# Performance work log

Measured on AMD Instinct MI355X. Metric: run time of the kernel, lower is better.

## Reference

```python
import jax, jax.numpy as jnp
import numpy as np

EXPAND = 2
KCONV = 4


def _mamba(x, Win, Wconv, bconv, Wx, Wdt, bdt, Alog, Dskip, Wout):
    # x: (B, C, H, W) -> flatten HW to a sequence, run Mamba (S6) block, reshape back
    B, C, H, W = x.shape
    L = H * W
    Di, Kc = Wconv.shape
    R = Wdt.shape[0]
    N = Alog.shape[1]
    xl = x.reshape(B, C, L).transpose(0, 2, 1)            # (B, L, C)
    xz = xl @ Win                                          # (B, L, 2*Di)
    xs, z = xz[..., :Di], xz[..., Di:]
    xt = xs.transpose(0, 2, 1)                             # (B, Di, L)
    xp = jnp.pad(xt, ((0, 0), (0, 0), (Kc - 1, 0)))        # causal depthwise conv1d
    conv = bconv[None, :, None]
    for k in range(Kc):
        conv = conv + Wconv[:, k][None, :, None] * xp[:, :, k:k + L]
    u = jax.nn.silu(conv).transpose(0, 2, 1)               # (B, L, Di)
    dbc = u @ Wx                                           # (B, L, R+2N)
    dt = jax.nn.softplus(dbc[..., :R] @ Wdt + bdt)         # (B, L, Di)
    Bm = dbc[..., R:R + N]                                 # (B, L, N)
    Cm = dbc[..., R + N:]                                  # (B, L, N)
    A = -jnp.exp(Alog)                                     # (Di, N)
    dA = jnp.exp(dt[..., None] * A)                        # (B, L, Di, N)
    dBx = dt[..., None] * Bm[:, :, None, :] * u[..., None] # (B, L, Di, N)

    def step(h, inp):
        a, bx, c = inp
        h = a * h + bx
        return h, jnp.einsum('bdn,bn->bd', h, c)

    h0 = jnp.zeros((B, Di, N), x.dtype)
    _, ys = jax.lax.scan(step, h0, (jnp.swapaxes(dA, 0, 1), jnp.swapaxes(dBx, 0, 1), jnp.swapaxes(Cm, 0, 1)))
    y = jnp.swapaxes(ys, 0, 1) + u * Dskip                 # (B, L, Di)
    y = y * jax.nn.silu(z)
    return (y @ Wout).transpose(0, 2, 1).reshape(B, C, H, W)


def _resize_bilinear(x, oh, ow):
    # F.interpolate(mode='bilinear', align_corners=True)
    B, C, H, W = x.shape
    ys = jnp.linspace(0.0, H - 1.0, oh)
    xs = jnp.linspace(0.0, W - 1.0, ow)
    y0 = jnp.floor(ys).astype(jnp.int32); y1 = jnp.clip(y0 + 1, 0, H - 1); wy = (ys - y0)[:, None]
    x0 = jnp.floor(xs).astype(jnp.int32); x1 = jnp.clip(x0 + 1, 0, W - 1); wx = (xs - x0)[None, :]
    r0 = x[:, :, y0, :]
    r1 = x[:, :, y1, :]
    top = r0[..., x0] * (1 - wx) + r0[..., x1] * wx
    bot = r1[..., x0] * (1 - wx) + r1[..., x1] * wx
    return top * (1 - wy) + bot * wy


def _mamba_params(key, D, N):
    Di = EXPAND * D
    R = max(1, D // 16)
    ks = jax.random.split(key, 6)
    s = 0.02
    Win = s * jax.random.normal(ks[0], (D, 2 * Di), jnp.float32)
    Wconv = s * jax.random.normal(ks[1], (Di, KCONV), jnp.float32)
    bconv = jnp.zeros((Di,), jnp.float32)
    Wx = s * jax.random.normal(ks[2], (Di, R + 2 * N), jnp.float32)
    Wdt = s * jax.random.normal(ks[3], (R, Di), jnp.float32)
    bdt = s * jax.random.normal(ks[4], (Di,), jnp.float32)
    Alog = jnp.tile(jnp.log(jnp.arange(1, N + 1, dtype=jnp.float32))[None, :], (Di, 1))
    Dskip = jnp.ones((Di,), jnp.float32)
    Wout = s * jax.random.normal(ks[5], (Di, D), jnp.float32)
    return Win, Wconv, bconv, Wx, Wdt, bdt, Alog, Dskip, Wout


def setup_inputs() -> dict:
    key = jax.random.key(0)
    C, B, N = 64, 2, 16
    sizes = [48, 24, 12, 6]
    ks = jax.random.split(key, 16)
    inp = {}
    for i, s in enumerate(sizes):
        inp[f'feat{i}'] = jax.random.normal(ks[i], (B, C, s, s), jnp.float32)
    names = ['Win', 'Wconv', 'bconv', 'Wx', 'Wdt', 'bdt', 'Alog', 'D', 'Wout']
    lvl = [_mamba_params(ks[4 + i], C, N) for i in range(4)]
    for j, nm in enumerate(names):
        inp['lvl_' + nm] = jnp.stack([lvl[i][j] for i in range(4)])
    cr = _mamba_params(ks[8], 4 * C, N)
    for j, nm in enumerate(names):
        inp['cr_' + nm] = cr[j]
    inp['proj_W'] = 0.02 * jax.random.normal(ks[9], (C, 4 * C), jnp.float32)  # 1x1 conv weight (out,in)
    inp['proj_b'] = jnp.zeros((C,), jnp.float32)
    inp['bn_g'] = jnp.ones((C,), jnp.float32)
    inp['bn_b'] = jnp.zeros((C,), jnp.float32)
    inp['bn_m'] = 0.1 * jax.random.normal(ks[10], (C,), jnp.float32)
    inp['bn_v'] = jax.random.uniform(ks[11], (C,), jnp.float32, minval=0.5, maxval=1.5)
    inp['target_h'] = 48
    inp['target_w'] = 48
    return inp


def reference(feat0, feat1, feat2, feat3,
              lvl_Win, lvl_Wconv, lvl_bconv, lvl_Wx, lvl_Wdt, lvl_bdt, lvl_Alog, lvl_D, lvl_Wout,
              cr_Win, cr_Wconv, cr_bconv, cr_Wx, cr_Wdt, cr_bdt, cr_Alog, cr_D, cr_Wout,
              proj_W, proj_b, bn_g, bn_b, bn_m, bn_v, target_h, target_w):
    feats = [feat0, feat1, feat2, feat3]
    processed = []
    for i, f in enumerate(feats):
        f = f + _mamba(f, lvl_Win[i], lvl_Wconv[i], lvl_bconv[i], lvl_Wx[i], lvl_Wdt[i],
                       lvl_bdt[i], lvl_Alog[i], lvl_D[i], lvl_Wout[i])
        processed.append(_resize_bilinear(f, target_h, target_w))
    x = jnp.concatenate(processed, axis=1)                 # (B, 4C, th, tw)
    x = x + _mamba(x, cr_Win, cr_Wconv, cr_bconv, cr_Wx, cr_Wdt, cr_bdt, cr_Alog, cr_D, cr_Wout)
    y = jnp.einsum('bchw,oc->bohw', x, proj_W) + proj_b[None, :, None, None]
    scale = (bn_g / jnp.sqrt(bn_v + 1e-5))[None, :, None, None]
    y = (y - bn_m[None, :, None, None]) * scale + bn_b[None, :, None, None]
    return jax.nn.relu(y)
```

## Files before the change

### kernel.cpp

```cpp
#include <hip/hip_runtime.h>
#include <cmath>

#define DEV __device__ __forceinline__

typedef unsigned short u16;
typedef u16 u16x8 __attribute__((ext_vector_type(8)));
typedef u16 u16x4 __attribute__((ext_vector_type(4)));
typedef short bf16x8 __attribute__((ext_vector_type(8)));
typedef float f32x4 __attribute__((ext_vector_type(4)));

constexpr int B_ = 2;
constexpr int S4[4]    = {48, 24, 12, 6};
constexpr int L4[4]    = {2304, 576, 144, 36};
constexpr int LOFF4[4] = {0, 2304, 2880, 3024};
constexpr int LTOT = 3060;
constexpr int TOFF4[4] = {0, 144, 180, 189};
constexpr int NTT = 192;
constexpr int NCH4[4]   = {36, 9, 3, 1};
constexpr int CHOFF4[4] = {0, 36, 45, 48};
constexpr int NCHL = 49;
constexpr int NCHC = 36;
constexpr int LC = 2304;
constexpr float LOG2E = 1.44269504088896f;

DEV float siluf(float x) { return x / (1.f + __expf(-x)); }
DEV float softplusf(float x) { return fmaxf(x, 0.f) + log1pf(__expf(-fabsf(x))); }
DEV float b2f(u16 x) { union { float f; unsigned u; } v; v.u = ((unsigned)x) << 16; return v.f; }
DEV u16 f2b(float f) {
  union { float f; unsigned u; } v; v.f = f;
  unsigned r = v.u + 0x7fffu + ((v.u >> 16) & 1u);
  return (u16)(r >> 16);
}

__global__ __launch_bounds__(256) void k_prep(
    const float* __restrict__ projW, const float* __restrict__ crWout,
    const float* __restrict__ cWin, const float* __restrict__ cWx,
    float* __restrict__ Wt, float* __restrict__ WP,
    u16* __restrict__ WinT, float* __restrict__ WxT) {
  __shared__ float sm[64 * 65];
  int blk = blockIdx.x;
  int tid = threadIdx.x;
  if (blk < 64) {
    int i = blk * 256 + tid;
    int o = i >> 8, c = i & 255;
    Wt[c * 64 + o] = projW[o * 256 + c];
  } else if (blk < 192) {
    int i = (blk - 64) * 256 + tid;
    int d = i >> 6, o = i & 63;
    float acc = 0.f;
#pragma unroll 4
    for (int c = 0; c < 256; ++c)
      acc = fmaf(crWout[d * 256 + c], projW[o * 256 + c], acc);
    WP[d * 64 + o] = acc;
  } else if (blk < 256) {
    int t = blk - 192;
    int ct = t & 3, nt = t >> 2;
    int c0 = ct * 64, n0 = nt * 64;
    for (int i = tid; i < 4096; i += 256) {
      int cc = i >> 6, nn = i & 63;
      sm[cc * 65 + nn] = cWin[(size_t)(c0 + cc) * 1024 + n0 + nn];
    }
    __syncthreads();
    for (int i = tid; i < 4096; i += 256) {
      int nn = i >> 6, cc = i & 63;
      WinT[(size_t)(n0 + nn) * 256 + c0 + cc] = f2b(sm[cc * 65 + nn]);
    }
  } else {
    int i = (blk - 256) * 256 + tid;
    int d = i & 511, j = i >> 9;
    WxT[j * 512 + d] = cWx[d * 48 + j];
  }
}

__global__ __launch_bounds__(256) void k_front_lvl(
    const float* __restrict__ f0, const float* __restrict__ f1,
    const float* __restrict__ f2, const float* __restrict__ f3,
    const float* __restrict__ Win,
    const float* __restrict__ Wconv,
    const float* __restrict__ bconv,
    const float* __restrict__ Wx,
    const float* __restrict__ Wdt,
    const float* __restrict__ bdt,
    u16* __restrict__ u_l, u16* __restrict__ dt_l,
    u16* __restrict__ Bm_l, u16* __restrict__ Cm_l, u16* __restrict__ z_l) {
  __shared__ float s_x[64 * 20];
  __shared__ float s_xs[19 * 128];
  __shared__ float s_u[16 * 132];
  __shared__ float s_dbc[16 * 36];
  int bid = blockIdx.x;
  int b = bid / NTT, t = bid - b * NTT;
  int lvl = 0;
  while (lvl < 3 && t >= TOFF4[lvl + 1]) ++lvl;
  int tl = t - TOFF4[lvl];
  int L = L4[lvl], loff = LOFF4[lvl];
  int l0 = tl * 16;
  int nl = min(16, L - l0);
  const float* fx = lvl == 0 ? f0 : lvl == 1 ? f1 : lvl == 2 ? f2 : f3;
  int tid = threadIdx.x;

  for (int i = tid; i < 64 * 20; i += 256) {
    int c = i / 20, r = i - c * 20;
    int l = l0 - 3 + r;
    float v = 0.f;
    if (r < 19 && l >= 0 && l < L) v = fx[(size_t)(b * 64 + c) * L + l];
    s_x[i] = v;
  }
  __syncthreads();
  {
    int j = tid;
    float acc[19];
#pragma unroll
    for (int r = 0; r < 19; ++r) acc[r] = 0.f;
    const float* W = Win + lvl * 64 * 256 + j;
    for (int c = 0; c < 64; ++c) {
      float w = W[c * 256];
#pragma unroll
      for (int r = 0; r < 19; ++r) acc[r] = fmaf(w, s_x[c * 20 + r], acc[r]);
    }
    if (j < 128) {
#pragma unroll
      for (int r = 0; r < 19; ++r) s_xs[r * 128 + j] = acc[r];
    } else {
      int d = j - 128;
      int dti = d >> 4, jj = d & 15;
      for (int r = 3; r < 19; ++r) {
        int l = l0 - 3 + r;
        if (l < l0 + nl)
          z_l[((size_t)(b * 8 + dti) * LTOT + loff + l) * 16 + jj] = f2b(acc[r]);
      }
    }
  }
  __syncthreads();
  for (int i = tid; i < 16 * 128; i += 256) {
    int l = i >> 7, d = i & 127;
    if (l < nl) {
      const float* wc = Wconv + (lvl * 128 + d) * 4;
      float a = bconv[lvl * 128 + d];
#pragma unroll
      for (int k = 0; k < 4; ++k) a = fmaf(wc[k], s_xs[(l + k) * 128 + d], a);
      float uu = siluf(a);
      s_u[l * 132 + d] = uu;
      u_l[((size_t)(b * 8 + (d >> 4)) * LTOT + loff + l0 + l) * 16 + (d & 15)] = f2b(uu);
    }
  }
  __syncthreads();
  for (int i = tid; i < 16 * 36; i += 256) {
    int l = i & 15, jj = i >> 4;
    if (l < nl) {
      const float* wx = Wx + lvl * 128 * 36 + jj;
      float a = 0.f;
      for (int d = 0; d < 128; ++d) a = fmaf(s_u[l * 132 + d], wx[d * 36], a);
      s_dbc[l * 36 + jj] = a;
      if (jj >= 4) {
        int q = jj - 4;
        size_t gb = ((size_t)(b * LTOT) + loff + l0 + l) * 16;
        if (q < 16) Bm_l[gb + q] = f2b(a);
        else        Cm_l[gb + (q - 16)] = f2b(a);
      }
    }
  }
  __syncthreads();
  for (int i = tid; i < 16 * 128; i += 256) {
    int l = i >> 7, d = i & 127;
    if (l < nl) {
      float a = bdt[lvl * 128 + d];
#pragma unroll
      for (int r = 0; r < 4; ++r)
        a = fmaf(s_dbc[l * 36 + r], Wdt[(lvl * 4 + r) * 128 + d], a);
      dt_l[((size_t)(b * 8 + (d >> 4)) * LTOT + loff + l0 + l) * 16 + (d & 15)] =
          f2b(softplusf(a));
    }
  }
}

template <int MODE, int PASSC>
__global__ __launch_bounds__(256) void k_scan(
    const u16* __restrict__ dtb, const u16* __restrict__ ub,
    const u16* __restrict__ Bmb, const u16* __restrict__ Cmb,
    const u16* __restrict__ zb,
    const float* __restrict__ Alog, const float* __restrict__ Dsk,
    float* __restrict__ hloc, float* __restrict__ Ssum,
    const float* __restrict__ hin, u16* __restrict__ yg) {
  constexpr int DI = MODE ? 512 : 128;
  constexpr int NDT = DI / 16;
  constexpr int NB = DI / 64;
  constexpr int NCHT = MODE ? NCHC : NCHL;
  constexpr int LT = MODE ? LC : LTOT;
  __shared__ __align__(16) u16 smem[PASSC ? 14336 : 9216];
  u16* s_dt = smem;
  u16* s_u  = smem + 4096;
  u16* s_B  = smem + 8192;
  u16* s_C  = PASSC ? smem + 9216 : nullptr;
  u16* s_y  = PASSC ? smem + 10240 : nullptr;

  int bid = blockIdx.x;
  int dblk = bid % NB;
  int rem = bid / NB;
  int gc = rem % NCHT;
  int b = rem / NCHT;
  int lvl = 0, ch = gc, Lq = LC, loff = 0;
  if (MODE == 0) {
    while (lvl < 3 && gc >= CHOFF4[lvl + 1]) ++lvl;
    ch = gc - CHOFF4[lvl];
    Lq = L4[lvl];
    loff = LOFF4[lvl];
  }
  int l0 = ch * 64;
  int len = min(64, Lq - l0);
  int labs0 = loff + l0;
  int tid = threadIdx.x;
  int q = tid & 3;
  int dl = (tid >> 2) & 15;
  int ti_l = tid >> 6;
  int dti = dblk * 4 + ti_l;
  int d = dti * 16 + dl;
  int n0 = q * 4;

  for (int ti = 0; ti < 4; ++ti) {
    size_t g2 = ((size_t)(b * NDT + dblk * 4 + ti) * LT + labs0) * 16;
    const u16x8* pdt = (const u16x8*)(dtb + g2);
    const u16x8* pu  = (const u16x8*)(ub + g2);
    for (int i = tid; i < len * 2; i += 256) {
      *(u16x8*)&s_dt[ti * 1024 + i * 8] = pdt[i];
      *(u16x8*)&s_u [ti * 1024 + i * 8] = pu[i];
    }
  }
  {
    size_t gB = ((size_t)b * LT + labs0) * 16;
    for (int i = tid; i < len * 2; i += 256) {
      *(u16x8*)&s_B[i * 8] = *(const u16x8*)&Bmb[gB + i * 8];
      if (PASSC) *(u16x8*)&s_C[i * 8] = *(const u16x8*)&Cmb[gB + i * 8];
    }
  }
  __syncthreads();

  int ai = (MODE ? d : lvl * 128 + d);
  float4 al = *(const float4*)&Alog[ai * 16 + n0];
  float kA2[4] = {-__expf(al.x) * LOG2E, -__expf(al.y) * LOG2E,
                  -__expf(al.z) * LOG2E, -__expf(al.w) * LOG2E};
  size_t hix = (((size_t)(b * NCHT) + gc) * DI + d) * 16 + n0;
  float h[4] = {0.f, 0.f, 0.f, 0.f};
  if (PASSC) {
    float4 hv = *(const float4*)&hin[hix];
    h[0] = hv.x; h[1] = hv.y; h[2] = hv.z; h[3] = hv.w;
  }
  float dsk = PASSC ? Dsk[ai] : 0.f;
  float ss = 0.f;

  for (int l = 0; l < len; ++l) {
    float dt = b2f(s_dt[ti_l * 1024 + l * 16 + dl]);
    float uu = b2f(s_u [ti_l * 1024 + l * 16 + dl]);
    float dtu = dt * uu;
    u16x4 Bv = *(const u16x4*)&s_B[l * 16 + n0];
    if (PASSC) {
      u16x4 Cv = *(const u16x4*)&s_C[l * 16 + n0];
      float p = 0.f;
#pragma unroll
      for (int i = 0; i < 4; ++i) {
        float dA = exp2f(kA2[i] * dt);
        h[i] = fmaf(dA, h[i], dtu * b2f(Bv[i]));
        p = fmaf(h[i], b2f(Cv[i]), p);
      }
      p += __shfl_xor(p, 1, 4);
      p += __shfl_xor(p, 2, 4);
      if (q == 0) s_y[l * 64 + ti_l * 16 + dl] = f2b(fmaf(uu, dsk, p));
    } else {
#pragma unroll
      for (int i = 0; i < 4; ++i) {
        float dA = exp2f(kA2[i] * dt);
        h[i] = fmaf(dA, h[i], dtu * b2f(Bv[i]));
      }
      ss += dt;
    }
  }
  if (!PASSC) {
    f32x4 hv = {h[0], h[1], h[2], h[3]};
    *(f32x4*)&hloc[hix] = hv;
    if (q == 0) Ssum[((size_t)(b * NCHT) + gc) * DI + d] = ss;
  } else {
    __syncthreads();
    for (int ti = 0; ti < 4; ++ti) {
      size_t g2 = ((size_t)(b * NDT + dblk * 4 + ti) * LT + labs0) * 16;
      for (int i = tid; i < len * 2; i += 256) {
        u16x8 zv = *(const u16x8*)&zb[g2 + i * 8];
        u16x8 yv = *(const u16x8*)&s_y[(i >> 1) * 64 + ti * 16 + (i & 1) * 8];
        u16x8 o;
#pragma unroll
        for (int j = 0; j < 8; ++j) {
          float z = b2f(zv[j]);
          float gate = z / (1.f + __expf(-z));
          o[j] = f2b(b2f(yv[j]) * gate);
        }
        *(u16x8*)&yg[g2 + i * 8] = o;
      }
    }
  }
}

__global__ __launch_bounds__(256) void k_combine_lvl(
    const float* __restrict__ Alog, const float* __restrict__ hloc,
    const float* __restrict__ Ssum, float* __restrict__ hin) {
  int i = blockIdx.x * 256 + threadIdx.x;
  int n = i & 15, d = (i >> 4) & 127, lvl = (i >> 11) & 3, b = i >> 13;
  float kA2 = -__expf(Alog[(lvl * 128 + d) * 16 + n]) * LOG2E;
  float h = 0.f;
  int nch = NCH4[lvl];
  for (int ch = 0; ch < nch; ++ch) {
    int gc = CHOFF4[lvl] + ch;
    size_t ix = (((size_t)(b * NCHL) + gc) * 128 + d) * 16 + n;
    hin[ix] = h;
    float S = Ssum[((size_t)(b * NCHL) + gc) * 128 + d];
    h = fmaf(exp2f(kA2 * S), h, hloc[ix]);
  }
}

__global__ __launch_bounds__(256) void k_combine_cr(
    const float* __restrict__ Alog, const float* __restrict__ hloc,
    const float* __restrict__ Ssum, float* __restrict__ hin) {
  int i = blockIdx.x * 256 + threadIdx.x;
  int n = i & 15, d = (i >> 4) & 511, b = i >> 13;
  float kA2 = -__expf(Alog[d * 16 + n]) * LOG2E;
  float h = 0.f;
  for (int ch = 0; ch < NCHC; ++ch) {
    size_t ix = (((size_t)(b * NCHC) + ch) * 512 + d) * 16 + n;
    hin[ix] = h;
    float S = Ssum[((size_t)(b * NCHC) + ch) * 512 + d];
    h = fmaf(exp2f(kA2 * S), h, hloc[ix]);
  }
}

__global__ __launch_bounds__(256) void k_out_lvl(
    const u16* __restrict__ yg_l, const float* __restrict__ Wout,
    const float* __restrict__ f0, const float* __restrict__ f1,
    const float* __restrict__ f2, const float* __restrict__ f3,
    float* __restrict__ fout) {
  __shared__ float s_ygT[128 * 20];
  __shared__ float s_o[16 * 64];
  int bid = blockIdx.x;
  int b = bid / NTT, t = bid - b * NTT;
  int lvl = 0;
  while (lvl < 3 && t >= TOFF4[lvl + 1]) ++lvl;
  int tl = t - TOFF4[lvl];
  int L = L4[lvl], loff = LOFF4[lvl];
  int l0 = tl * 16, nl = min(16, L - l0);
  const float* fx = lvl == 0 ? f0 : lvl == 1 ? f1 : lvl == 2 ? f2 : f3;
  int tid = threadIdx.x;
  for (int i = tid; i < 16 * 128; i += 256) {
    int d = i & 127, l = i >> 7;
    float v = 0.f;
    if (l < nl)
      v = b2f(yg_l[((size_t)(b * 8 + (d >> 4)) * LTOT + loff + l0 + l) * 16 + (d & 15)]);
    s_ygT[d * 20 + l] = v;
  }
  __syncthreads();
  {
    int c = tid & 63, lg = (tid >> 6) * 4;
    float acc[4] = {0.f, 0.f, 0.f, 0.f};
    const float* W = Wout + lvl * 128 * 64 + c;
    for (int dq = 0; dq < 128; ++dq) {
      float w = W[dq * 64];
      float4 yv = *(const float4*)&s_ygT[dq * 20 + lg];
      acc[0] = fmaf(w, yv.x, acc[0]);
      acc[1] = fmaf(w, yv.y, acc[1]);
      acc[2] = fmaf(w, yv.z, acc[2]);
      acc[3] = fmaf(w, yv.w, acc[3]);
    }
#pragma unroll
    for (int a = 0; a < 4; ++a) s_o[(lg + a) * 64 + c] = acc[a];
  }
  __syncthreads();
  for (int i = tid; i < 16 * 64; i += 256) {
    int c = i >> 4, l = i & 15;
    if (l < nl)
      fout[((size_t)(b * 64) + c) * LTOT + loff + l0 + l] =
          s_o[l * 64 + c] + fx[((size_t)(b * 64) + c) * L + l0 + l];
  }
}

__global__ __launch_bounds__(256) void k_resize(const float* __restrict__ fout,
                                                float* __restrict__ xTf,
                                                u16* __restrict__ xTb) {
  int i = blockIdx.x * 256 + threadIdx.x;
  int ch = i & 255;
  int rem = i >> 8;
  int hw = rem % 2304;
  int b = rem / 2304;
  int oh = hw / 48, ow = hw - oh * 48;
  int lvl = ch >> 6, c = ch & 63;
  int s = S4[lvl];
  const float* base = fout + ((size_t)(b * 64) + c) * LTOT + LOFF4[lvl];
  float scl = (float)(s - 1) * (1.f / 47.f);
  float fy = oh * scl, fxx = ow * scl;
  int y0 = (int)floorf(fy), x0 = (int)floorf(fxx);
  float wy = fy - y0, wx = fxx - x0;
  int y1 = min(y0 + 1, s - 1), x1 = min(x0 + 1, s - 1);
  float v00 = base[y0 * s + x0], v01 = base[y0 * s + x1];
  float v10 = base[y1 * s + x0], v11 = base[y1 * s + x1];
  float top = v00 * (1.f - wx) + v01 * wx;
  float bot = v10 * (1.f - wx) + v11 * wx;
  float v = top * (1.f - wy) + bot * wy;
  xTf[i] = v;
  xTb[i] = f2b(v);
}

__global__ __launch_bounds__(256) void k_gemm_mfma(
    const u16* __restrict__ xT,
    const u16* __restrict__ WT,
    u16* __restrict__ xs_c, u16* __restrict__ z_c) {
  __shared__ __align__(16) u16 s_a[64 * 72];
  __shared__ __align__(16) u16 s_b[128 * 72];
  int bid = blockIdx.x;
  int nj = bid & 7, bm = bid >> 3;
  int tid = threadIdx.x;
  int lane = tid & 63, w = tid >> 6;
  int wm = (w & 1) * 32, wn = (w >> 1) * 64;
  const int m_base = bm * 64;
  const int n_base = nj * 128;

  f32x4 acc[2][4];
#pragma unroll
  for (int mi = 0; mi < 2; ++mi)
#pragma unroll
    for (int ni = 0; ni < 4; ++ni) acc[mi][ni] = {0.f, 0.f, 0.f, 0.f};

  u16x8 ra0, ra1, rb0, rb1, rb2, rb3;
  auto ld = [&](int c0) {
#pragma unroll
    for (int s = 0; s < 2; ++s) {
      int v = s * 256 + tid;
      int row = v >> 3, kc = (v & 7) * 8;
      u16x8 t = *(const u16x8*)&xT[(size_t)(m_base + row) * 256 + c0 + kc];
      if (s == 0) ra0 = t; else ra1 = t;
    }
#pragma unroll
    for (int s = 0; s < 4; ++s) {
      int v = s * 256 + tid;
      int row = v >> 3, kc = (v & 7) * 8;
      u16x8 t = *(const u16x8*)&WT[(size_t)(n_base + row) * 256 + c0 + kc];
      if (s == 0) rb0 = t; else if (s == 1) rb1 = t;
      else if (s == 2) rb2 = t; else rb3 = t;
    }
  };
  auto st = [&]() {
#pragma unroll
    for (int s = 0; s < 2; ++s) {
      int v = s * 256 + tid;
      int row = v >> 3, kc = (v & 7) * 8;
      *(u16x8*)&s_a[row * 72 + kc] = (s == 0) ? ra0 : ra1;
    }
#pragma unroll
    for (int s = 0; s < 4; ++s) {
      int v = s * 256 + tid;
      int row = v >> 3, kc = (v & 7) * 8;
      const u16x8& t = (s == 0) ? rb0 : (s == 1) ? rb1 : (s == 2) ? rb2 : rb3;
      *(u16x8*)&s_b[row * 72 + kc] = t;
    }
  };
  ld(0);
  int mlane = lane & 15, kg = (lane >> 4) * 8;
  for (int kt = 0; kt < 4; ++kt) {
    st();
    __syncthreads();
    if (kt < 3) ld((kt + 1) * 64);
#pragma unroll
    for (int kk = 0; kk < 2; ++kk) {
      int k0 = kk * 32 + kg;
      bf16x8 af[2], bfr[4];
#pragma unroll
      for (int mi = 0; mi < 2; ++mi)
        af[mi] = *(const bf16x8*)&s_a[(wm + mi * 16 + mlane) * 72 + k0];
#pragma unroll
      for (int ni = 0; ni < 4; ++ni)
        bfr[ni] = *(const bf16x8*)&s_b[(wn + ni * 16 + mlane) * 72 + k0];
#pragma unroll
      for (int mi = 0; mi < 2; ++mi)
#pragma unroll
        for (int ni = 0; ni < 4; ++ni)
          acc[mi][ni] = __builtin_amdgcn_mfma_f32_16x16x32_bf16(
              af[mi], bfr[ni], acc[mi][ni], 0, 0, 0);
    }
    __syncthreads();
  }
  int rgrp = (lane >> 4) * 4;
#pragma unroll
  for (int mi = 0; mi < 2; ++mi) {
#pragma unroll
    for (int ni = 0; ni < 4; ++ni) {
      int n = n_base + wn + ni * 16 + mlane;
#pragma unroll
      for (int r = 0; r < 4; ++r) {
        int gm = m_base + wm + mi * 16 + rgrp + r;
        int b = gm >= 2304;
        int l = gm - b * 2304;
        u16 v = f2b(acc[mi][ni][r]);
        if (n < 512) {
          xs_c[((size_t)(b * LC) + l) * 512 + n] = v;
        } else {
          int dz = n - 512;
          z_c[((size_t)(b * 32 + (dz >> 4)) * LC + l) * 16 + (dz & 15)] = v;
        }
      }
    }
  }
}

__global__ __launch_bounds__(1024) void k_mid_cr(
    const u16* __restrict__ xs_c,
    const float* __restrict__ Wconv,
    const float* __restrict__ bconv,
    const float* __restrict__ WxT,
    const float* __restrict__ Wdt,
    const float* __restrict__ bdt, u16* __restrict__ u_c,
    u16* __restrict__ dt_c, u16* __restrict__ Bm_c, u16* __restrict__ Cm_c) {
  __shared__ __align__(16) u16 s_xs[19 * 512];
  __shared__ __align__(16) u16 s_ub[16 * 520];
  __shared__ __align__(16) float s_wx[48 * 132];
  __shared__ float s_dbc[16 * 48];
  int bid = blockIdx.x;
  int b = bid / 144, tl = bid - b * 144;
  int l0 = tl * 16;
  int tid = threadIdx.x;
  for (int i = tid; i < 19 * 64; i += 1024) {
    int r = i >> 6, c8 = (i & 63) * 8;
    int l = l0 - 3 + r;
    u16x8 v = {0, 0, 0, 0, 0, 0, 0, 0};
    if (l >= 0)
      v = *(const u16x8*)&xs_c[((size_t)(b * LC) + l) * 512 + c8];
    *(u16x8*)&s_xs[r * 512 + c8] = v;
  }
  __syncthreads();
  for (int i = tid; i < 16 * 512; i += 1024) {
    int l = i >> 9, d = i & 511;
    const float* wc = Wconv + d * 4;
    float a = bconv[d];
#pragma unroll
    for (int k = 0; k < 4; ++k) a = fmaf(wc[k], b2f(s_xs[(l + k) * 512 + d]), a);
    float uu = siluf(a);
    u16 ub = f2b(uu);
    s_ub[l * 520 + d] = ub;
    u_c[((size_t)(b * 32 + (d >> 4)) * LC + l0 + l) * 16 + (d & 15)] = ub;
  }
  int dl = tid & 15, jj = tid >> 4;
  float a8[8] = {0.f, 0.f, 0.f, 0.f, 0.f, 0.f, 0.f, 0.f};
  for (int kt = 0; kt < 4; ++kt) {
    __syncthreads();
    for (int i = tid; i < 1536; i += 1024) {
      int row = i >> 5, c4 = (i & 31) * 4;
      *(float4*)&s_wx[row * 132 + c4] =
          *(const float4*)&WxT[row * 512 + kt * 128 + c4];
    }
    __syncthreads();
    if (tid < 768) {
      const u16* ur = s_ub + dl * 520 + kt * 128;
      const float* wr = s_wx + jj * 132;
#pragma unroll 4
      for (int kb = 0; kb < 16; ++kb) {
        u16x8 uv = *(const u16x8*)&ur[kb * 8];
        float4 w0 = *(const float4*)&wr[kb * 8];
        float4 w1 = *(const float4*)&wr[kb * 8 + 4];
        a8[0] = fmaf(b2f(uv[0]), w0.x, a8[0]);
        a8[1] = fmaf(b2f(uv[1]), w0.y, a8[1]);
        a8[2] = fmaf(b2f(uv[2]), w0.z, a8[2]);
        a8[3] = fmaf(b2f(uv[3]), w0.w, a8[3]);
        a8[4] = fmaf(b2f(uv[4]), w1.x, a8[4]);
        a8[5] = fmaf(b2f(uv[5]), w1.y, a8[5]);
        a8[6] = fmaf(b2f(uv[6]), w1.z, a8[6]);
        a8[7] = fmaf(b2f(uv[7]), w1.w, a8[7]);
      }
    }
  }
  if (tid < 768) {
    float a = ((a8[0] + a8[1]) + (a8[2] + a8[3])) +
              ((a8[4] + a8[5]) + (a8[6] + a8[7]));
    s_dbc[dl * 48 + jj] = a;
    if (jj >= 16) {
      int q = jj - 16;
      size_t gb = ((size_t)(b * LC) + l0 + dl) * 16;
      if (q < 16) Bm_c[gb + q] = f2b(a);
      else        Cm_c[gb + (q - 16)] = f2b(a);
    }
  }
  __syncthreads();
  for (int i = tid; i < 16 * 512; i += 1024) {
    int l = i >> 9, d = i & 511;
    float a = bdt[d];
#pragma unroll
    for (int r = 0; r < 16; ++r)
      a = fmaf(s_dbc[l * 48 + r], Wdt[r * 512 + d], a);
    dt_c[((size_t)(b * 32 + (d >> 4)) * LC + l0 + l) * 16 + (d & 15)] =
        f2b(softplusf(a));
  }
}

__global__ __launch_bounds__(256) void k_final(
    const float* __restrict__ xTf, const u16* __restrict__ yg_c,
    const float* __restrict__ Wt, const float* __restrict__ WP,
    const float* __restrict__ pb, const float* __restrict__ bng,
    const float* __restrict__ bnb, const float* __restrict__ bnm,
    const float* __restrict__ bnv, float* __restrict__ out) {
  __shared__ float s_xc[256 * 8];
  __shared__ float s_yg[512 * 8];
  __shared__ float s_w[32 * 64];
  int bid = blockIdx.x;
  int b = bid / 288, tl = bid - b * 288;
  int l0 = tl * 8;
  int tid = threadIdx.x;
  for (int i = tid; i < 2048; i += 256) {
    int c = i & 255, l = i >> 8;
    s_xc[c * 8 + l] = xTf[((size_t)(b * 2304) + l0 + l) * 256 + c];
  }
  for (int i = tid; i < 4096; i += 256) {
    int j = i & 15, l = (i >> 4) & 7, dt = i >> 7;
    s_yg[(dt * 16 + j) * 8 + l] =
        b2f(yg_c[((size_t)(b * 32 + dt) * LC + l0 + l) * 16 + j]);
  }
  int o = tid & 63, lg = (tid >> 6) * 2;
  float acc0 = 0.f, acc1 = 0.f;
  float4 r0, r1;
  auto ldT = [&](const float* W, int kt, float4& a0, float4& a1) {
#pragma unroll
    for (int s = 0; s < 2; ++s) {
      int idx = s * 256 + tid;
      int row = idx >> 4, c4 = (idx & 15) << 2;
      float4 v = *(const float4*)&W[(kt * 32 + row) * 64 + c4];
      if (s == 0) a0 = v; else a1 = v;
    }
  };
  auto stT = [&](const float4& a0, const float4& a1) {
#pragma unroll
    for (int s = 0; s < 2; ++s) {
      int idx = s * 256 + tid;
      int row = idx >> 4, c4 = (idx & 15) << 2;
      *(float4*)&s_w[row * 64 + c4] = (s == 0) ? a0 : a1;
    }
  };
  ldT(Wt, 0, r0, r1);
  __syncthreads();
  stT(r0, r1);
  __syncthreads();
  for (int kt = 0; kt < 8; ++kt) {
    if (kt < 7) ldT(Wt, kt + 1, r0, r1);
    else ldT(WP, 0, r0, r1);
#pragma unroll
    for (int cc = 0; cc < 32; ++cc) {
      float w = s_w[cc * 64 + o];
      float2 xv = *(const float2*)&s_xc[(kt * 32 + cc) * 8 + lg];
      acc0 = fmaf(w, xv.x, acc0);
      acc1 = fmaf(w, xv.y, acc1);
    }
    __syncthreads();
    stT(r0, r1);
    __syncthreads();
  }
  for (int kt = 0; kt < 16; ++kt) {
    if (kt < 15) ldT(WP, kt + 1, r0, r1);
#pragma unroll
    for (int cc = 0; cc < 32; ++cc) {
      float w = s_w[cc * 64 + o];
      float2 yv = *(const float2*)&s_yg[(kt * 32 + cc) * 8 + lg];
      acc0 = fmaf(w, yv.x, acc0);
      acc1 = fmaf(w, yv.y, acc1);
    }
    __syncthreads();
    if (kt < 15) {
      stT(r0, r1);
      __syncthreads();
    }
  }
  float bias = pb[o], m = bnm[o], g = bng[o], v = bnv[o], bb = bnb[o];
  float scl = g * (1.f / sqrtf(v + 1e-5f));
  float2 r;
  r.x = fmaxf((acc0 + bias - m) * scl + bb, 0.f);
  r.y = fmaxf((acc1 + bias - m) * scl + bb, 0.f);
  *(float2*)&out[((size_t)(b * 64) + o) * LC + l0 + lg] = r;
}

extern "C" void kernel_launch(void* const* d_in, const int* in_sizes, int n_in,
                              void* d_out, int out_size, void* d_ws,
                              size_t ws_size, hipStream_t stream) {
  (void)in_sizes; (void)n_in; (void)out_size; (void)ws_size;
  const float* f0 = (const float*)d_in[0];
  const float* f1 = (const float*)d_in[1];
  const float* f2 = (const float*)d_in[2];
  const float* f3 = (const float*)d_in[3];
  const float* lWin   = (const float*)d_in[4];
  const float* lWconv = (const float*)d_in[5];
  const float* lbconv = (const float*)d_in[6];
  const float* lWx    = (const float*)d_in[7];
  const float* lWdt   = (const float*)d_in[8];
  const float* lbdt   = (const float*)d_in[9];
  const float* lAlog  = (const float*)d_in[10];
  const float* lD     = (const float*)d_in[11];
  const float* lWout  = (const float*)d_in[12];
  const float* cWin   = (const float*)d_in[13];
  const float* cWconv = (const float*)d_in[14];
  const float* cbconv = (const float*)d_in[15];
  const float* cWx    = (const float*)d_in[16];
  const float* cWdt   = (const float*)d_in[17];
  const float* cbdt   = (const float*)d_in[18];
  const float* cAlog  = (const float*)d_in[19];
  const float* cD     = (const float*)d_in[20];
  const float* cWout  = (const float*)d_in[21];
  const float* projW  = (const float*)d_in[22];
  const float* projb  = (const float*)d_in[23];
  const float* bng    = (const float*)d_in[24];
  const float* bnb    = (const float*)d_in[25];
  const float* bnm    = (const float*)d_in[26];
  const float* bnv    = (const float*)d_in[27];
  float* out = (float*)d_out;

  float* ws = (float*)d_ws;
  size_t off = 0;
  auto allocf = [&](size_t n) { float* p = ws + off; off += (n + 7) & ~(size_t)7; return p; };
  auto allocb = [&](size_t n) { u16* p = (u16*)(ws + off); off += ((n + 1) / 2 + 7) & ~(size_t)7; return p; };

  float* Wt     = allocf(256 * 64);
  float* WP     = allocf(512 * 64);
  float* WxT    = allocf(48 * 512);
  float* fout   = allocf((size_t)B_ * 64 * LTOT);
  float* xTf    = allocf((size_t)B_ * LC * 256);
  float* hloc_l = allocf((size_t)B_ * NCHL * 128 * 16);
  float* S_l    = allocf((size_t)B_ * NCHL * 128);
  float* hin_l  = allocf((size_t)B_ * NCHL * 128 * 16);
  float* hloc_c = allocf((size_t)B_ * NCHC * 512 * 16);
  float* S_c    = allocf((size_t)B_ * NCHC * 512);
  float* hin_c  = allocf((size_t)B_ * NCHC * 512 * 16);

  u16* WinT  = allocb(1024 * 256);
  u16* xTb   = allocb((size_t)B_ * LC * 256);
  u16* u_l2  = allocb((size_t)B_ * 8 * LTOT * 16);
  u16* dt_l2 = allocb((size_t)B_ * 8 * LTOT * 16);
  u16* z_l2  = allocb((size_t)B_ * 8 * LTOT * 16);
  u16* yg_l2 = allocb((size_t)B_ * 8 * LTOT * 16);
  u16* Bm_l2 = allocb((size_t)B_ * LTOT * 16);
  u16* Cm_l2 = allocb((size_t)B_ * LTOT * 16);
  u16* xs_c2 = allocb((size_t)B_ * LC * 512);
  u16* u_c2  = allocb((size_t)B_ * 32 * LC * 16);
  u16* dt_c2 = allocb((size_t)B_ * 32 * LC * 16);
  u16* z_c2  = allocb((size_t)B_ * 32 * LC * 16);
  u16* yg_c2 = allocb((size_t)B_ * 32 * LC * 16);
  u16* Bm_c2 = allocb((size_t)B_ * LC * 16);
  u16* Cm_c2 = allocb((size_t)B_ * LC * 16);

  k_prep<<<352, 256, 0, stream>>>(projW, cWout, cWin, cWx, Wt, WP, WinT, WxT);

  k_front_lvl<<<B_ * NTT, 256, 0, stream>>>(f0, f1, f2, f3, lWin, lWconv,
                                            lbconv, lWx, lWdt, lbdt, u_l2,
                                            dt_l2, Bm_l2, Cm_l2, z_l2);

  k_scan<0, 0><<<B_ * NCHL * 2, 256, 0, stream>>>(
      dt_l2, u_l2, Bm_l2, Cm_l2, nullptr, lAlog, lD, hloc_l, S_l, nullptr,
      nullptr);
  k_combine_lvl<<<64, 256, 0, stream>>>(lAlog, hloc_l, S_l, hin_l);
  k_scan<0, 1><<<B_ * NCHL * 2, 256, 0, stream>>>(
      dt_l2, u_l2, Bm_l2, Cm_l2, z_l2, lAlog, lD, nullptr, nullptr, hin_l,
      yg_l2);

  k_out_lvl<<<B_ * NTT, 256, 0, stream>>>(yg_l2, lWout, f0, f1, f2, f3, fout);
  k_resize<<<(B_ * 256 * LC) / 256, 256, 0, stream>>>(fout, xTf, xTb);

  k_gemm_mfma<<<72 * 8, 256, 0, stream>>>(xTb, WinT, xs_c2, z_c2);
  k_mid_cr<<<B_ * 144, 1024, 0, stream>>>(xs_c2, cWconv, cbconv, WxT, cWdt,
                                          cbdt, u_c2, dt_c2, Bm_c2, Cm_c2);

  k_scan<1, 0><<<B_ * NCHC * 8, 256, 0, stream>>>(
      dt_c2, u_c2, Bm_c2, Cm_c2, nullptr, cAlog, cD, hloc_c, S_c, nullptr,
      nullptr);
  k_combine_cr<<<64, 256, 0, stream>>>(cAlog, hloc_c, S_c, hin_c);
  k_scan<1, 1><<<B_ * NCHC * 8, 256, 0, stream>>>(
      dt_c2, u_c2, Bm_c2, Cm_c2, z_c2, cAlog, cD, nullptr, nullptr, hin_c,
      yg_c2);

  k_final<<<B_ * 288, 256, 0, stream>>>(xTf, yg_c2, Wt, WP, projb, bng, bnb,
                                        bnm, bnv, out);
}
```

Before: 342.9 us.

## Use MFMA bf16 for final projection and halve scan chunk length

```diff
diff --git a/kernel.cpp b/kernel.cpp
--- a/kernel.cpp
+++ b/kernel.cpp
@@ -16,10 +16,10 @@
 constexpr int LTOT = 3060;
 constexpr int TOFF4[4] = {0, 144, 180, 189};
 constexpr int NTT = 192;
-constexpr int NCH4[4]   = {36, 9, 3, 1};
-constexpr int CHOFF4[4] = {0, 36, 45, 48};
-constexpr int NCHL = 49;
-constexpr int NCHC = 36;
+constexpr int NCH4[4]   = {72, 18, 5, 2};
+constexpr int CHOFF4[4] = {0, 72, 90, 95};
+constexpr int NCHL = 97;
+constexpr int NCHC = 72;
 constexpr int LC = 2304;
 constexpr float LOG2E = 1.44269504088896f;
 
@@ -35,23 +35,22 @@
 __global__ __launch_bounds__(256) void k_prep(
     const float* __restrict__ projW, const float* __restrict__ crWout,
     const float* __restrict__ cWin, const float* __restrict__ cWx,
-    float* __restrict__ Wt, float* __restrict__ WP,
+    u16* __restrict__ WPB, u16* __restrict__ WtB,
     u16* __restrict__ WinT, float* __restrict__ WxT) {
   __shared__ float sm[64 * 65];
   int blk = blockIdx.x;
   int tid = threadIdx.x;
-  if (blk < 64) {
+  if (blk < 128) {
     int i = blk * 256 + tid;
-    int o = i >> 8, c = i & 255;
-    Wt[c * 64 + o] = projW[o * 256 + c];
-  } else if (blk < 192) {
-    int i = (blk - 64) * 256 + tid;
     int d = i >> 6, o = i & 63;
     float acc = 0.f;
 #pragma unroll 4
     for (int c = 0; c < 256; ++c)
       acc = fmaf(crWout[d * 256 + c], projW[o * 256 + c], acc);
-    WP[d * 64 + o] = acc;
+    WPB[o * 512 + d] = f2b(acc);
+  } else if (blk < 192) {
+    int i = (blk - 128) * 256 + tid;
+    WtB[i] = f2b(projW[i]);
   } else if (blk < 256) {
     int t = blk - 192;
     int ct = t & 3, nt = t >> 2;
@@ -186,12 +185,12 @@
   constexpr int NB = DI / 64;
   constexpr int NCHT = MODE ? NCHC : NCHL;
   constexpr int LT = MODE ? LC : LTOT;
-  __shared__ __align__(16) u16 smem[PASSC ? 14336 : 9216];
+  __shared__ __align__(16) u16 smem[PASSC ? 7168 : 4608];
   u16* s_dt = smem;
-  u16* s_u  = smem + 4096;
-  u16* s_B  = smem + 8192;
-  u16* s_C  = PASSC ? smem + 9216 : nullptr;
-  u16* s_y  = PASSC ? smem + 10240 : nullptr;
+  u16* s_u  = smem + 2048;
+  u16* s_B  = smem + 4096;
+  u16* s_C  = PASSC ? smem + 4608 : nullptr;
+  u16* s_y  = PASSC ? smem + 5120 : nullptr;
 
   int bid = blockIdx.x;
   int dblk = bid % NB;
@@ -205,8 +204,8 @@
     Lq = L4[lvl];
     loff = LOFF4[lvl];
   }
-  int l0 = ch * 64;
-  int len = min(64, Lq - l0);
+  int l0 = ch * 32;
+  int len = min(32, Lq - l0);
   int labs0 = loff + l0;
   int tid = threadIdx.x;
   int q = tid & 3;
@@ -221,8 +220,8 @@
     const u16x8* pdt = (const u16x8*)(dtb + g2);
     const u16x8* pu  = (const u16x8*)(ub + g2);
     for (int i = tid; i < len * 2; i += 256) {
-      *(u16x8*)&s_dt[ti * 1024 + i * 8] = pdt[i];
-      *(u16x8*)&s_u [ti * 1024 + i * 8] = pu[i];
+      *(u16x8*)&s_dt[ti * 512 + i * 8] = pdt[i];
+      *(u16x8*)&s_u [ti * 512 + i * 8] = pu[i];
     }
   }
   {
@@ -248,8 +247,8 @@
   float ss = 0.f;
 
   for (int l = 0; l < len; ++l) {
-    float dt = b2f(s_dt[ti_l * 1024 + l * 16 + dl]);
-    float uu = b2f(s_u [ti_l * 1024 + l * 16 + dl]);
+    float dt = b2f(s_dt[ti_l * 512 + l * 16 + dl]);
+    float uu = b2f(s_u [ti_l * 512 + l * 16 + dl]);
     float dtu = dt * uu;
     u16x4 Bv = *(const u16x4*)&s_B[l * 16 + n0];
     if (PASSC) {
@@ -378,7 +377,6 @@
 }
 
 __global__ __launch_bounds__(256) void k_resize(const float* __restrict__ fout,
-                                                float* __restrict__ xTf,
                                                 u16* __restrict__ xTb) {
   int i = blockIdx.x * 256 + threadIdx.x;
   int ch = i & 255;
@@ -398,9 +396,7 @@
   float v10 = base[y1 * s + x0], v11 = base[y1 * s + x1];
   float top = v00 * (1.f - wx) + v01 * wx;
   float bot = v10 * (1.f - wx) + v11 * wx;
-  float v = top * (1.f - wy) + bot * wy;
-  xTf[i] = v;
-  xTb[i] = f2b(v);
+  xTb[i] = f2b(top * (1.f - wy) + bot * wy);
 }
 
 __global__ __launch_bounds__(256) void k_gemm_mfma(
@@ -592,87 +588,59 @@
   }
 }
 
-__global__ __launch_bounds__(256) void k_final(
-    const float* __restrict__ xTf, const u16* __restrict__ yg_c,
-    const float* __restrict__ Wt, const float* __restrict__ WP,
+__global__ __launch_bounds__(64) void k_final_mfma(
+    const u16* __restrict__ xTb,
+    const u16* __restrict__ yg_c,
+    const u16* __restrict__ WtB,
+    const u16* __restrict__ WPB,
     const float* __restrict__ pb, const float* __restrict__ bng,
     const float* __restrict__ bnb, const float* __restrict__ bnm,
     const float* __restrict__ bnv, float* __restrict__ out) {
-  __shared__ float s_xc[256 * 8];
-  __shared__ float s_yg[512 * 8];
-  __shared__ float s_w[32 * 64];
-  int bid = blockIdx.x;
-  int b = bid / 288, tl = bid - b * 288;
-  int l0 = tl * 8;
-  int tid = threadIdx.x;
-  for (int i = tid; i < 2048; i += 256) {
-    int c = i & 255, l = i >> 8;
-    s_xc[c * 8 + l] = xTf[((size_t)(b * 2304) + l0 + l) * 256 + c];
-  }
-  for (int i = tid; i < 4096; i += 256) {
-    int j = i & 15, l = (i >> 4) & 7, dt = i >> 7;
-    s_yg[(dt * 16 + j) * 8 + l] =
-        b2f(yg_c[((size_t)(b * 32 + dt) * LC + l0 + l) * 16 + j]);
-  }
-  int o = tid & 63, lg = (tid >> 6) * 2;
-  float acc0 = 0.f, acc1 = 0.f;
-  float4 r0, r1;
-  auto ldT = [&](const float* W, int kt, float4& a0, float4& a1) {
-#pragma unroll
-    for (int s = 0; s < 2; ++s) {
-      int idx = s * 256 + tid;
-      int row = idx >> 4, c4 = (idx & 15) << 2;
-      float4 v = *(const float4*)&W[(kt * 32 + row) * 64 + c4];
-      if (s == 0) a0 = v; else a1 = v;
-    }
-  };
-  auto stT = [&](const float4& a0, const float4& a1) {
-#pragma unroll
-    for (int s = 0; s < 2; ++s) {
-      int idx = s * 256 + tid;
-      int row = idx >> 4, c4 = (idx & 15) << 2;
-      *(float4*)&s_w[row * 64 + c4] = (s == 0) ? a0 : a1;
-    }
-  };
-  ldT(Wt, 0, r0, r1);
-  __syncthreads();
-  stT(r0, r1);
-  __syncthreads();
+  int bm = blockIdx.x;
+  int b = bm >= 144;
+  int m_base = bm * 16;
+  int l_base = m_base - b * 2304;
+  int lane = threadIdx.x;
+  int mrow = lane & 15;
+  int kg = (lane >> 4) * 8;
+  f32x4 acc[4];
+#pragma unroll
+  for (int ni = 0; ni < 4; ++ni) acc[ni] = {0.f, 0.f, 0.f, 0.f};
+#pragma unroll
   for (int kt = 0; kt < 8; ++kt) {
-    if (kt < 7) ldT(Wt, kt + 1, r0, r1);
-    else ldT(WP, 0, r0, r1);
-#pragma unroll
-    for (int cc = 0; cc < 32; ++cc) {
-      float w = s_w[cc * 64 + o];
-      float2 xv = *(const float2*)&s_xc[(kt * 32 + cc) * 8 + lg];
-      acc0 = fmaf(w, xv.x, acc0);
-      acc1 = fmaf(w, xv.y, acc1);
-    }
-    __syncthreads();
-    stT(r0, r1);
-    __syncthreads();
-  }
+    int k0 = kt * 32;
+    bf16x8 af = *(const bf16x8*)&xTb[(size_t)(m_base + mrow) * 256 + k0 + kg];
+#pragma unroll
+    for (int ni = 0; ni < 4; ++ni) {
+      bf16x8 bw = *(const bf16x8*)&WtB[(ni * 16 + mrow) * 256 + k0 + kg];
+      acc[ni] = __builtin_amdgcn_mfma_f32_16x16x32_bf16(af, bw, acc[ni], 0, 0, 0);
+    }
+  }
+#pragma unroll
   for (int kt = 0; kt < 16; ++kt) {
-    if (kt < 15) ldT(WP, kt + 1, r0, r1);
-#pragma unroll
-    for (int cc = 0; cc < 32; ++cc) {
-      float w = s_w[cc * 64 + o];
-      float2 yv = *(const float2*)&s_yg[(kt * 32 + cc) * 8 + lg];
-      acc0 = fmaf(w, yv.x, acc0);
-      acc1 = fmaf(w, yv.y, acc1);
-    }
-    __syncthreads();
-    if (kt < 15) {
-      stT(r0, r1);
-      __syncthreads();
-    }
-  }
-  float bias = pb[o], m = bnm[o], g = bng[o], v = bnv[o], bb = bnb[o];
-  float scl = g * (1.f / sqrtf(v + 1e-5f));
-  float2 r;
-  r.x = fmaxf((acc0 + bias - m) * scl + bb, 0.f);
-  r.y = fmaxf((acc1 + bias - m) * scl + bb, 0.f);
-  *(float2*)&out[((size_t)(b * 64) + o) * LC + l0 + lg] = r;
+    int kp = kt * 32 + kg;
+    int dt = kp >> 4, j0 = kp & 15;
+    bf16x8 af = *(const bf16x8*)
+        &yg_c[((size_t)(b * 32 + dt) * LC + l_base + mrow) * 16 + j0];
+#pragma unroll
+    for (int ni = 0; ni < 4; ++ni) {
+      bf16x8 bw = *(const bf16x8*)&WPB[(ni * 16 + mrow) * 512 + kt * 32 + kg];
+      acc[ni] = __builtin_amdgcn_mfma_f32_16x16x32_bf16(af, bw, acc[ni], 0, 0, 0);
+    }
+  }
+  int rg = (lane >> 4) * 4;
+#pragma unroll
+  for (int ni = 0; ni < 4; ++ni) {
+    int o = ni * 16 + mrow;
+    float bias = pb[o], m = bnm[o], g = bng[o], v = bnv[o], bb2 = bnb[o];
+    float scl = g * (1.f / sqrtf(v + 1e-5f));
+    float4 r;
+    r.x = fmaxf((acc[ni][0] + bias - m) * scl + bb2, 0.f);
+    r.y = fmaxf((acc[ni][1] + bias - m) * scl + bb2, 0.f);
+    r.z = fmaxf((acc[ni][2] + bias - m) * scl + bb2, 0.f);
+    r.w = fmaxf((acc[ni][3] + bias - m) * scl + bb2, 0.f);
+    *(float4*)&out[((size_t)(b * 64) + o) * LC + l_base + rg] = r;
+  }
 }
 
 extern "C" void kernel_launch(void* const* d_in, const int* in_sizes, int n_in,
@@ -714,11 +682,8 @@
   auto allocf = [&](size_t n) { float* p = ws + off; off += (n + 7) & ~(size_t)7; return p; };
   auto allocb = [&](size_t n) { u16* p = (u16*)(ws + off); off += ((n + 1) / 2 + 7) & ~(size_t)7; return p; };
 
-  float* Wt     = allocf(256 * 64);
-  float* WP     = allocf(512 * 64);
   float* WxT    = allocf(48 * 512);
   float* fout   = allocf((size_t)B_ * 64 * LTOT);
-  float* xTf    = allocf((size_t)B_ * LC * 256);
   float* hloc_l = allocf((size_t)B_ * NCHL * 128 * 16);
   float* S_l    = allocf((size_t)B_ * NCHL * 128);
   float* hin_l  = allocf((size_t)B_ * NCHL * 128 * 16);
@@ -726,6 +691,8 @@
   float* S_c    = allocf((size_t)B_ * NCHC * 512);
   float* hin_c  = allocf((size_t)B_ * NCHC * 512 * 16);
 
+  u16* WPB   = allocb(64 * 512);
+  u16* WtB   = allocb(64 * 256);
   u16* WinT  = allocb(1024 * 256);
   u16* xTb   = allocb((size_t)B_ * LC * 256);
   u16* u_l2  = allocb((size_t)B_ * 8 * LTOT * 16);
@@ -742,7 +709,7 @@
   u16* Bm_c2 = allocb((size_t)B_ * LC * 16);
   u16* Cm_c2 = allocb((size_t)B_ * LC * 16);
 
-  k_prep<<<352, 256, 0, stream>>>(projW, cWout, cWin, cWx, Wt, WP, WinT, WxT);
+  k_prep<<<352, 256, 0, stream>>>(projW, cWout, cWin, cWx, WPB, WtB, WinT, WxT);
 
   k_front_lvl<<<B_ * NTT, 256, 0, stream>>>(f0, f1, f2, f3, lWin, lWconv,
                                             lbconv, lWx, lWdt, lbdt, u_l2,
@@ -757,7 +724,7 @@
       yg_l2);
 
   k_out_lvl<<<B_ * NTT, 256, 0, stream>>>(yg_l2, lWout, f0, f1, f2, f3, fout);
-  k_resize<<<(B_ * 256 * LC) / 256, 256, 0, stream>>>(fout, xTf, xTb);
+  k_resize<<<(B_ * 256 * LC) / 256, 256, 0, stream>>>(fout, xTb);
 
   k_gemm_mfma<<<72 * 8, 256, 0, stream>>>(xTb, WinT, xs_c2, z_c2);
   k_mid_cr<<<B_ * 144, 1024, 0, stream>>>(xs_c2, cWconv, cbconv, WxT, cWdt,
@@ -771,6 +738,6 @@
       dt_c2, u_c2, Bm_c2, Cm_c2, z_c2, cAlog, cD, nullptr, nullptr, hin_c,
       yg_c2);
 
-  k_final<<<B_ * 288, 256, 0, stream>>>(xTf, yg_c2, Wt, WP, projb, bng, bnb,
-                                        bnm, bnv, out);
-}
+  k_final_mfma<<<288, 64, 0, stream>>>(xTb, yg_c2, WtB, WPB, projb, bng, bnb,
+                                       bnm, bnv, out);
+}
```

Result: faster. 315.8 us (-7.9%).
